# Optimization experiments

Measured on AMD Instinct MI355X. Metric: run time of the kernel, lower is better.

Reference implementation:

```python
import jax, jax.numpy as jnp
import numpy as np

EPS = 1e-12  # torch F.normalize eps

def _l2norm(x):
    # F.normalize(x, p=2, dim=-1): x / max(||x||_2, eps)
    n = jnp.sqrt(jnp.sum(x * x, axis=-1, keepdims=True))
    return x / jnp.maximum(n, EPS)

def setup_inputs() -> dict:
    key = jax.random.key(0)
    k1, k2, k3 = jax.random.split(key, 3)
    B, N, D = 8, 8192, 512
    return {
        "s": jax.random.normal(k1, (B, N, D), dtype=jnp.float32),
        "h_rl": jax.random.normal(k2, (B, N, D), dtype=jnp.float32),
        "h_fk": jax.random.normal(k3, (B, N, D), dtype=jnp.float32),
    }

def reference(s, h_rl, h_fk):
    # diagonal(bmm(s, h^T)) == row-wise dot product; compute it directly
    s_n = _l2norm(s)
    sc_rl = jnp.sum(s_n * _l2norm(h_rl), axis=-1)  # [B, N]
    sc_fk = jnp.sum(s_n * _l2norm(h_fk), axis=-1)  # [B, N]
    return jnp.concatenate((sc_rl, sc_fk), axis=1)  # [B, 2N]
```

## Files before the change

kernel.cpp:

```cpp
#include <hip/hip_runtime.h>

#define DIM 512
#define NPB 8192

__device__ __forceinline__ float dot4(float4 u, float4 v) {
    return u.x * v.x + u.y * v.y + u.z * v.z + u.w * v.w;
}

__global__ __launch_bounds__(256) void disc_kernel(
    const float* __restrict__ s,
    const float* __restrict__ hrl,
    const float* __restrict__ hfk,
    float* __restrict__ out,
    int n_rows) {
    int gid  = blockIdx.x * blockDim.x + threadIdx.x;
    int row  = gid >> 6;
    int lane = threadIdx.x & 63;
    if (row >= n_rows) return;

    size_t base = (size_t)row * DIM;
    const float4* sp = (const float4*)(s + base);
    const float4* ap = (const float4*)(hrl + base);
    const float4* bp = (const float4*)(hfk + base);

    float4 s0 = sp[lane];
    float4 s1 = sp[lane + 64];
    float4 a0 = ap[lane];
    float4 a1 = ap[lane + 64];
    float4 b0 = bp[lane];
    float4 b1 = bp[lane + 64];

    float ss = dot4(s0, s0) + dot4(s1, s1);
    float aa = dot4(a0, a0) + dot4(a1, a1);
    float bb = dot4(b0, b0) + dot4(b1, b1);
    float sa = dot4(s0, a0) + dot4(s1, a1);
    float sb = dot4(s0, b0) + dot4(s1, b1);

    #pragma unroll
    for (int off = 32; off > 0; off >>= 1) {
        ss += __shfl_down(ss, off, 64);
        aa += __shfl_down(aa, off, 64);
        bb += __shfl_down(bb, off, 64);
        sa += __shfl_down(sa, off, 64);
        sb += __shfl_down(sb, off, 64);
    }

    if (lane == 0) {
        const float eps = 1e-12f;
        float ns = fmaxf(sqrtf(ss), eps);
        float na = fmaxf(sqrtf(aa), eps);
        float nb = fmaxf(sqrtf(bb), eps);
        int bidx = row / NPB;
        int n    = row & (NPB - 1);
        size_t obase = (size_t)bidx * (2 * NPB) + n;
        out[obase]       = sa / (ns * na);
        out[obase + NPB] = sb / (ns * nb);
    }
}

extern "C" void kernel_launch(void* const* d_in, const int* in_sizes, int n_in,
                              void* d_out, int out_size, void* d_ws, size_t ws_size,
                              hipStream_t stream) {
    const float* s   = (const float*)d_in[0];
    const float* hrl = (const float*)d_in[1];
    const float* hfk = (const float*)d_in[2];
    float* out = (float*)d_out;

    int n_rows = in_sizes[0] / DIM;
    int threads = 256;
    int waves_per_block = threads / 64;
    int blocks = (n_rows + waves_per_block - 1) / waves_per_block;

    disc_kernel<<<blocks, threads, 0, stream>>>(s, hrl, hfk, out, n_rows);
}
```

Baseline: 347.3 us.

## Use persistent grid-stride waves with register prefetch and nontemporal loads

```diff
diff --git a/kernel.cpp b/kernel.cpp
--- a/kernel.cpp
+++ b/kernel.cpp
@@ -3,8 +3,15 @@
 #define DIM 512
 #define NPB 8192
 
-__device__ __forceinline__ float dot4(float4 u, float4 v) {
-    return u.x * v.x + u.y * v.y + u.z * v.z + u.w * v.w;
+typedef float f4 __attribute__((ext_vector_type(4)));
+
+__device__ __forceinline__ float dot4(f4 u, f4 v) {
+    f4 p = u * v;
+    return p.x + p.y + p.z + p.w;
+}
+
+__device__ __forceinline__ f4 ntload(const f4* p) {
+    return __builtin_nontemporal_load(p);
 }
 
 __global__ __launch_bounds__(256) void disc_kernel(
@@ -12,49 +19,61 @@
     const float* __restrict__ hrl,
     const float* __restrict__ hfk,
     float* __restrict__ out,
-    int n_rows) {
-    int gid  = blockIdx.x * blockDim.x + threadIdx.x;
-    int row  = gid >> 6;
+    int n_rows, int total_waves) {
+    int wave = (blockIdx.x * blockDim.x + threadIdx.x) >> 6;
     int lane = threadIdx.x & 63;
+
+    int row = wave;
     if (row >= n_rows) return;
 
-    size_t base = (size_t)row * DIM;
-    const float4* sp = (const float4*)(s + base);
-    const float4* ap = (const float4*)(hrl + base);
-    const float4* bp = (const float4*)(hfk + base);
+    const f4* sp = (const f4*)(s   + (size_t)row * DIM);
+    const f4* ap = (const f4*)(hrl + (size_t)row * DIM);
+    const f4* bp = (const f4*)(hfk + (size_t)row * DIM);
+    f4 s0 = ntload(sp + lane), s1 = ntload(sp + lane + 64);
+    f4 a0 = ntload(ap + lane), a1 = ntload(ap + lane + 64);
+    f4 b0 = ntload(bp + lane), b1 = ntload(bp + lane + 64);
 
-    float4 s0 = sp[lane];
-    float4 s1 = sp[lane + 64];
-    float4 a0 = ap[lane];
-    float4 a1 = ap[lane + 64];
-    float4 b0 = bp[lane];
-    float4 b1 = bp[lane + 64];
+    while (row < n_rows) {
+        int nrow = row + total_waves;
+        f4 t0, t1, u0, u1, v0, v1;
+        if (nrow < n_rows) {
+            const f4* spn = (const f4*)(s   + (size_t)nrow * DIM);
+            const f4* apn = (const f4*)(hrl + (size_t)nrow * DIM);
+            const f4* bpn = (const f4*)(hfk + (size_t)nrow * DIM);
+            t0 = ntload(spn + lane); t1 = ntload(spn + lane + 64);
+            u0 = ntload(apn + lane); u1 = ntload(apn + lane + 64);
+            v0 = ntload(bpn + lane); v1 = ntload(bpn + lane + 64);
+        }
 
-    float ss = dot4(s0, s0) + dot4(s1, s1);
-    float aa = dot4(a0, a0) + dot4(a1, a1);
-    float bb = dot4(b0, b0) + dot4(b1, b1);
-    float sa = dot4(s0, a0) + dot4(s1, a1);
-    float sb = dot4(s0, b0) + dot4(s1, b1);
+        float ss = dot4(s0, s0) + dot4(s1, s1);
+        float aa = dot4(a0, a0) + dot4(a1, a1);
+        float bb = dot4(b0, b0) + dot4(b1, b1);
+        float sa = dot4(s0, a0) + dot4(s1, a1);
+        float sb = dot4(s0, b0) + dot4(s1, b1);
 
-    #pragma unroll
-    for (int off = 32; off > 0; off >>= 1) {
-        ss += __shfl_down(ss, off, 64);
-        aa += __shfl_down(aa, off, 64);
-        bb += __shfl_down(bb, off, 64);
-        sa += __shfl_down(sa, off, 64);
-        sb += __shfl_down(sb, off, 64);
-    }
+        #pragma unroll
+        for (int off = 32; off > 0; off >>= 1) {
+            ss += __shfl_xor(ss, off, 64);
+            aa += __shfl_xor(aa, off, 64);
+            bb += __shfl_xor(bb, off, 64);
+            sa += __shfl_xor(sa, off, 64);
+            sb += __shfl_xor(sb, off, 64);
+        }
 
-    if (lane == 0) {
-        const float eps = 1e-12f;
-        float ns = fmaxf(sqrtf(ss), eps);
-        float na = fmaxf(sqrtf(aa), eps);
-        float nb = fmaxf(sqrtf(bb), eps);
-        int bidx = row / NPB;
-        int n    = row & (NPB - 1);
-        size_t obase = (size_t)bidx * (2 * NPB) + n;
-        out[obase]       = sa / (ns * na);
-        out[obase + NPB] = sb / (ns * nb);
+        if (lane == 0) {
+            const float eps = 1e-12f;
+            float ns = fmaxf(sqrtf(ss), eps);
+            float na = fmaxf(sqrtf(aa), eps);
+            float nb = fmaxf(sqrtf(bb), eps);
+            int bidx = row >> 13;
+            int n    = row & (NPB - 1);
+            size_t obase = (size_t)bidx * (2 * NPB) + n;
+            out[obase]       = sa / (ns * na);
+            out[obase + NPB] = sb / (ns * nb);
+        }
+
+        s0 = t0; s1 = t1; a0 = u0; a1 = u1; b0 = v0; b1 = v1;
+        row = nrow;
     }
 }
 
@@ -68,8 +87,8 @@
 
     int n_rows = in_sizes[0] / DIM;
     int threads = 256;
-    int waves_per_block = threads / 64;
-    int blocks = (n_rows + waves_per_block - 1) / waves_per_block;
+    int blocks  = 2048;
+    int total_waves = blocks * (threads / 64);
 
-    disc_kernel<<<blocks, threads, 0, stream>>>(s, hrl, hfk, out, n_rows);
+    disc_kernel<<<blocks, threads, 0, stream>>>(s, hrl, hfk, out, n_rows, total_waves);
 }
```

Result: faster. 324.1 us (-6.7%).
